# Kernel tuning notes

Hardware: AMD Instinct MI355X
Metric: run time of the kernel (lower is better)

## Reference

```python
import jax, jax.numpy as jnp
import numpy as np

N, E, ET = 50000, 400000, 50000
F, ED, H, L = 64, 32, 128, 2


def _forward(x, edge_attr, target_edge_attr, node_W, node_b, edge_W, edge_b,
             pre_W, pre_b, post_W, post_b, lin_W, lin_b, bn_g, bn_b,
             em1_W, em1_b, em2_W, em2_b, edge_index):
    n = x.shape[0]
    h = node_W.shape[1]
    src, dst = edge_index[0], edge_index[1]
    x = x @ node_W + node_b                      # [N,H]
    ea = edge_attr @ edge_W + edge_b             # [E,H]
    tea = target_edge_attr @ edge_W + edge_b     # [Et,H]

    ones = jnp.ones((src.shape[0],), jnp.float32)
    cnt = jax.ops.segment_sum(ones, dst, num_segments=n)        # in-degree per node
    avg_deg_log = jnp.mean(jnp.log(cnt + 1.0))                  # PyG avg_deg['log'] from deg histogram
    deg = jnp.clip(cnt, 1.0)[:, None]
    amp = jnp.log(deg + 1.0) / avg_deg_log                      # 'amplification' scaler
    att = avg_deg_log / jnp.log(deg + 1.0)                      # 'attenuation' scaler
    cnt_c = jnp.clip(cnt, 1.0)[:, None]
    has = (cnt > 0)[:, None]

    nlayers = pre_W.shape[0]
    for i in range(nlayers):
        # pre-MLP on message cat([x_i(dst), x_j(src), edge_attr]); split matmul avoids [E,3H] concat
        Wd, Ws, We = pre_W[i, :h], pre_W[i, h:2 * h], pre_W[i, 2 * h:]
        m = x[dst] @ Wd + x[src] @ Ws + ea @ We + pre_b[i]      # [E,H]
        s = jax.ops.segment_sum(m, dst, num_segments=n)
        mean = s / cnt_c
        mean2 = jax.ops.segment_sum(m * m, dst, num_segments=n) / cnt_c
        std = jnp.sqrt(jax.nn.relu(mean2 - mean * mean) + 1e-5)  # PyG StdAggregation
        mn = jnp.where(has, jax.ops.segment_min(m, dst, num_segments=n), 0.0)
        mx = jnp.where(has, jax.ops.segment_max(m, dst, num_segments=n), 0.0)
        agg = jnp.concatenate([mean, mn, mx, std], axis=-1)     # [N,4H] aggregator order
        scaled = jnp.concatenate([agg, agg * amp, agg * att], axis=-1)  # [N,12H] scaler order
        # post-MLP on cat([x, scaled]); split matmul
        out = x @ post_W[i, :h] + scaled @ post_W[i, h:] + post_b[i]
        out = out @ lin_W[i] + lin_b[i]
        # BatchNorm (training mode, biased var, eps=1e-5)
        mu = out.mean(axis=0)
        var = jnp.mean((out - mu) ** 2, axis=0)
        bn = bn_g[i] * (out - mu) / jnp.sqrt(var + 1e-5) + bn_b[i]
        x = (x + jax.nn.relu(bn)) / 2
        # edge update: ea + MLP(cat([x[src], x[dst], ea])) / 2
        W1s, W1d, W1e = em1_W[i, :h], em1_W[i, h:2 * h], em1_W[i, 2 * h:]
        hid = jax.nn.relu(x[src] @ W1s + x[dst] @ W1d + ea @ W1e + em1_b[i])
        ea = ea + (hid @ em2_W[i] + em2_b[i]) / 2
    return (x, ea, tea)


def setup_inputs() -> dict:
    key = jax.random.key(0)
    ks = jax.random.split(key, 24)

    def w(k, shape):
        fan_in = shape[-2]
        return (jax.random.normal(k, shape, jnp.float32) / np.sqrt(fan_in)).astype(jnp.float32)

    inp = {
        'x': jax.random.normal(ks[0], (N, F), jnp.float32),
        'edge_attr': jax.random.normal(ks[1], (E, ED), jnp.float32),
        'target_edge_attr': jax.random.normal(ks[2], (ET, ED), jnp.float32),
        'node_W': w(ks[3], (F, H)), 'node_b': jnp.zeros((H,), jnp.float32),
        'edge_W': w(ks[4], (ED, H)), 'edge_b': jnp.zeros((H,), jnp.float32),
        'pre_W': w(ks[5], (L, 3 * H, H)), 'pre_b': jnp.zeros((L, H), jnp.float32),
        'post_W': w(ks[6], (L, 13 * H, H)), 'post_b': jnp.zeros((L, H), jnp.float32),
        'lin_W': w(ks[7], (L, H, H)), 'lin_b': jnp.zeros((L, H), jnp.float32),
        'bn_g': jnp.ones((L, H), jnp.float32), 'bn_b': jnp.zeros((L, H), jnp.float32),
        'em1_W': w(ks[8], (L, 3 * H, H)), 'em1_b': jnp.zeros((L, H), jnp.float32),
        'em2_W': w(ks[9], (L, H, H)), 'em2_b': jnp.zeros((L, H), jnp.float32),
        'edge_index': jax.random.randint(ks[10], (2, E), 0, N, dtype=jnp.int32),
    }
    return inp


def reference(x, edge_attr, target_edge_attr, node_W, node_b, edge_W, edge_b,
              pre_W, pre_b, post_W, post_b, lin_W, lin_b, bn_g, bn_b,
              em1_W, em1_b, em2_W, em2_b, edge_index):
    return _forward(x, edge_attr, target_edge_attr, node_W, node_b, edge_W, edge_b,
                    pre_W, pre_b, post_W, post_b, lin_W, lin_b, bn_g, bn_b,
                    em1_W, em1_b, em2_W, em2_b, edge_index)
```

## Files before the change

### kernel.cpp

```cpp
#include <hip/hip_runtime.h>
#include <math.h>

#define NN  50000
#define NE  400000
#define NTE 50000
#define FIN 64
#define EDIM 32
#define HD  128
#define NL  2
#define SCAN_B ((NN + 255) / 256)

typedef __attribute__((ext_vector_type(8))) short bf16x8;
typedef __attribute__((ext_vector_type(4))) short bf16x4;
typedef __attribute__((ext_vector_type(4))) float f32x4;

static __device__ __forceinline__ unsigned short f2bf(float f) {
    unsigned u = __float_as_uint(f);
    unsigned r = (u + 0x7fffu + ((u >> 16) & 1u)) >> 16;
    return (unsigned short)r;
}
static __device__ __forceinline__ float bfhi2f(unsigned u) { return __uint_as_float(u & 0xffff0000u); }
static __device__ __forceinline__ float bflo2f(unsigned u) { return __uint_as_float(u << 16); }

static __device__ __forceinline__ bf16x8 load_a8(const float* p, bool ok) {
    bf16x8 a = {};
    if (ok) {
        const float4 v0 = *(const float4*)(p);
        const float4 v1 = *(const float4*)(p + 4);
        a[0] = (short)f2bf(v0.x); a[1] = (short)f2bf(v0.y);
        a[2] = (short)f2bf(v0.z); a[3] = (short)f2bf(v0.w);
        a[4] = (short)f2bf(v1.x); a[5] = (short)f2bf(v1.y);
        a[6] = (short)f2bf(v1.z); a[7] = (short)f2bf(v1.w);
    }
    return a;
}
static __device__ __forceinline__ bf16x8 pack8(float4 a, float4 b) {
    bf16x8 v;
    v[0]=(short)f2bf(a.x); v[1]=(short)f2bf(a.y); v[2]=(short)f2bf(a.z); v[3]=(short)f2bf(a.w);
    v[4]=(short)f2bf(b.x); v[5]=(short)f2bf(b.y); v[6]=(short)f2bf(b.z); v[7]=(short)f2bf(b.w);
    return v;
}
static __device__ __forceinline__ bf16x4 pack4(float4 a) {
    bf16x4 v;
    v[0]=(short)f2bf(a.x); v[1]=(short)f2bf(a.y); v[2]=(short)f2bf(a.z); v[3]=(short)f2bf(a.w);
    return v;
}

__global__ void __launch_bounds__(256) k_packW(const float* __restrict__ W,
        unsigned short* __restrict__ out, int K)
{
    const int tid = blockIdx.x * 256 + threadIdx.x;
    const int total = (K / 32) * 512;
    if (tid >= total) return;
    const int lane = tid & 63, nt = (tid >> 6) & 7, kb = tid >> 9;
    const int k0 = kb * 32 + (lane >> 4) * 8;
    const int col = nt * 16 + (lane & 15);
    bf16x8 v;
    #pragma unroll
    for (int j = 0; j < 8; ++j)
        v[j] = (short)f2bf(W[(size_t)(k0 + j) * HD + col]);
    *(bf16x8*)(out + (size_t)tid * 8) = v;
}

template<int KB>
__global__ void __launch_bounds__(256) k_gemm_mfma(const float* A,
        const unsigned short* __restrict__ Wpk, const float* __restrict__ bias,
        float* C, int M)
{
    const int t = threadIdx.x, w = t >> 6, l = t & 63;
    const int row0 = blockIdx.x * 64 + w * 16;
    const int ar = row0 + (l & 15);
    const bool aok = ar < M;
    const int kq = (l >> 4) * 8;
    const int K = KB * 32;
    f32x4 acc[8] = {};
    #pragma unroll
    for (int kb = 0; kb < KB; ++kb) {
        const bf16x8 a = load_a8(A + (size_t)ar * K + kb * 32 + kq, aok);
        #pragma unroll
        for (int nt = 0; nt < 8; ++nt) {
            const bf16x8 b = *(const bf16x8*)(Wpk + (((size_t)(kb * 8 + nt) * 64 + l) << 3));
            acc[nt] = __builtin_amdgcn_mfma_f32_16x16x32_bf16(a, b, acc[nt], 0, 0, 0);
        }
    }
    #pragma unroll
    for (int nt = 0; nt < 8; ++nt) {
        const int col = nt * 16 + (l & 15);
        const float bv = bias ? bias[col] : 0.f;
        #pragma unroll
        for (int r = 0; r < 4; ++r) {
            const int orow = row0 + (l >> 4) * 4 + r;
            if (orow < M) C[(size_t)orow * HD + col] = acc[nt][r] + bv;
        }
    }
}

template<int KB>
__global__ void __launch_bounds__(256) k_gemm2_mfma(const float* A,
        const unsigned short* __restrict__ W0, const unsigned short* __restrict__ W1,
        const float* __restrict__ b0, float* C0, float* C1, int M)
{
    const int t = threadIdx.x, w = t >> 6, l = t & 63;
    const int row0 = blockIdx.x * 64 + w * 16;
    const int ar = row0 + (l & 15);
    const bool aok = ar < M;
    const int kq = (l >> 4) * 8;
    const int K = KB * 32;
    f32x4 a0[8] = {}, a1[8] = {};
    #pragma unroll
    for (int kb = 0; kb < KB; ++kb) {
        const bf16x8 a = load_a8(A + (size_t)ar * K + kb * 32 + kq, aok);
        #pragma unroll
        for (int nt = 0; nt < 8; ++nt) {
            const bf16x8 u = *(const bf16x8*)(W0 + (((size_t)(kb * 8 + nt) * 64 + l) << 3));
            const bf16x8 v = *(const bf16x8*)(W1 + (((size_t)(kb * 8 + nt) * 64 + l) << 3));
            a0[nt] = __builtin_amdgcn_mfma_f32_16x16x32_bf16(a, u, a0[nt], 0, 0, 0);
            a1[nt] = __builtin_amdgcn_mfma_f32_16x16x32_bf16(a, v, a1[nt], 0, 0, 0);
        }
    }
    #pragma unroll
    for (int nt = 0; nt < 8; ++nt) {
        const int col = nt * 16 + (l & 15);
        const float bv = b0 ? b0[col] : 0.f;
        #pragma unroll
        for (int r = 0; r < 4; ++r) {
            const int orow = row0 + (l >> 4) * 4 + r;
            if (orow < M) {
                C0[(size_t)orow * HD + col] = a0[nt][r] + bv;
                C1[(size_t)orow * HD + col] = a1[nt][r];
            }
        }
    }
}

__global__ void __launch_bounds__(256) k_count(const int* __restrict__ d, int* __restrict__ cnt, int E)
{
    const int e = blockIdx.x * 256 + threadIdx.x;
    if (e < E) atomicAdd(&cnt[d[e]], 1);
}

__global__ void __launch_bounds__(256) k_avglog(const int* __restrict__ cnt, float* __restrict__ stats)
{
    float s = 0.f;
    for (int n = blockIdx.x * 256 + threadIdx.x; n < NN; n += gridDim.x * 256)
        s += logf((float)cnt[n] + 1.f);
    #pragma unroll
    for (int off = 32; off > 0; off >>= 1) s += __shfl_down(s, off);
    __shared__ float ls[4];
    if ((threadIdx.x & 63) == 0) ls[threadIdx.x >> 6] = s;
    __syncthreads();
    if (threadIdx.x == 0) unsafeAtomicAdd(stats, ls[0] + ls[1] + ls[2] + ls[3]);
}

__global__ void __launch_bounds__(256) k_scan_block(const int* __restrict__ cnt,
        int* __restrict__ incl, int* __restrict__ part)
{
    __shared__ int s[256];
    const int t = threadIdx.x;
    const int i = blockIdx.x * 256 + t;
    const int v = (i < NN) ? cnt[i] : 0;
    s[t] = v;
    __syncthreads();
    #pragma unroll
    for (int off = 1; off < 256; off <<= 1) {
        const int x = (t >= off) ? s[t - off] : 0;
        __syncthreads();
        s[t] += x;
        __syncthreads();
    }
    if (i < NN) incl[i] = s[t];
    if (t == 255) part[blockIdx.x] = s[255];
}

__global__ void __launch_bounds__(256) k_scan_part(const int* __restrict__ part,
        int* __restrict__ poff, int np)
{
    __shared__ int s[256];
    const int t = threadIdx.x;
    const int v = (t < np) ? part[t] : 0;
    s[t] = v;
    __syncthreads();
    #pragma unroll
    for (int off = 1; off < 256; off <<= 1) {
        const int x = (t >= off) ? s[t - off] : 0;
        __syncthreads();
        s[t] += x;
        __syncthreads();
    }
    poff[t] = s[t] - v;
}

__global__ void __launch_bounds__(256) k_scan_add(const int* __restrict__ incl,
        const int* __restrict__ cnt, const int* __restrict__ poff,
        int* __restrict__ row_start, int* __restrict__ cursor)
{
    const int i = blockIdx.x * 256 + threadIdx.x;
    if (i < NN) {
        const int excl = incl[i] - cnt[i] + poff[blockIdx.x];
        row_start[i] = excl;
        cursor[i] = excl;
    }
    if (i == 0) row_start[NN] = NE;
}

__global__ void __launch_bounds__(256) k_scatter(const int* __restrict__ dstp,
        int* cursor, int* __restrict__ sppos)
{
    const int e = blockIdx.x * 256 + threadIdx.x;
    if (e < NE) sppos[e] = atomicAdd(&cursor[dstp[e]], 1);
}

__global__ void __launch_bounds__(256) k_msg_T(const float* __restrict__ ea,
        const unsigned short* __restrict__ Wepk, const float* __restrict__ xs,
        const int* __restrict__ srcp, const int* __restrict__ sppos,
        unsigned short* __restrict__ mbuf)
{
    const int t = threadIdx.x, w = t >> 6, l = t & 63;
    const int e = blockIdx.x * 64 + w * 16 + (l & 15);
    const int q = l >> 4, kq = q * 8;
    f32x4 acc[8] = {};
    #pragma unroll
    for (int kb = 0; kb < 4; ++kb) {
        const bf16x8 bea = load_a8(ea + (size_t)e * HD + kb * 32 + kq, true);
        #pragma unroll
        for (int nt = 0; nt < 8; ++nt) {
            const bf16x8 aW = *(const bf16x8*)(Wepk + (((size_t)(kb * 8 + nt) * 64 + l) << 3));
            acc[nt] = __builtin_amdgcn_mfma_f32_16x16x32_bf16(aW, bea, acc[nt], 0, 0, 0);
        }
    }
    const int sn = srcp[e], sp = sppos[e];
    const float* ps = xs + (size_t)sn * HD + q * 4;
    unsigned short* pm = mbuf + (size_t)sp * HD + q * 4;
    #pragma unroll
    for (int nt = 0; nt < 8; ++nt) {
        const float4 sv = *(const float4*)(ps + nt * 16);
        float4 o;
        o.x = acc[nt][0] + sv.x; o.y = acc[nt][1] + sv.y;
        o.z = acc[nt][2] + sv.z; o.w = acc[nt][3] + sv.w;
        *(bf16x4*)(pm + nt * 16) = pack4(o);
    }
}

__global__ void __launch_bounds__(256) k_agg(const unsigned short* __restrict__ mbuf,
        const int* __restrict__ rs, const float* __restrict__ xd,
        unsigned short* __restrict__ aggb)
{
    const int n = blockIdx.x * 4 + (threadIdx.x >> 6);
    if (n >= NN) return;
    const int lane = threadIdx.x & 63;
    const int c = lane * 2;
    const int s = rs[n], e = rs[n + 1];
    const float2 xv = *(const float2*)(xd + (size_t)n * HD + c);
    float s0=0.f, s1=0.f, q0=0.f, q1=0.f;
    float mn0=INFINITY, mn1=INFINITY, mx0=-INFINITY, mx1=-INFINITY;
    for (int i = s; i < e; ++i) {
        const unsigned u = *(const unsigned*)(mbuf + (size_t)i * HD + c);
        const float v0 = bflo2f(u), v1 = bfhi2f(u);
        s0 += v0; s1 += v1;
        q0 += v0 * v0; q1 += v1 * v1;
        mn0 = fminf(mn0, v0); mn1 = fminf(mn1, v1);
        mx0 = fmaxf(mx0, v0); mx1 = fmaxf(mx1, v1);
    }
    const int deg = e - s;
    const float inv = 1.f / (float)(deg > 1 ? deg : 1);
    const float fd = (float)deg * inv;
    const float m0p = s0 * inv, m1p = s1 * inv;
    const float sd0 = sqrtf(fmaxf(q0 * inv - m0p * m0p, 0.f) + 1e-5f);
    const float sd1 = sqrtf(fmaxf(q1 * inv - m1p * m1p, 0.f) + 1e-5f);
    const bool has = deg > 0;
    const float mean0 = m0p + fd * xv.x, mean1 = m1p + fd * xv.y;
    const float omn0 = has ? mn0 + xv.x : 0.f, omn1 = has ? mn1 + xv.y : 0.f;
    const float omx0 = has ? mx0 + xv.x : 0.f, omx1 = has ? mx1 + xv.y : 0.f;
    unsigned* a = (unsigned*)(aggb + (size_t)n * 512 + c);
    a[0]         = (unsigned)f2bf(mean0) | ((unsigned)f2bf(mean1) << 16);
    *(a + 64)    = (unsigned)f2bf(omn0)  | ((unsigned)f2bf(omn1)  << 16);
    *(a + 128)   = (unsigned)f2bf(omx0)  | ((unsigned)f2bf(omx1)  << 16);
    *(a + 192)   = (unsigned)f2bf(sd0)   | ((unsigned)f2bf(sd1)   << 16);
}

__global__ void __launch_bounds__(256) k_post_lin(const float* __restrict__ x,
        const unsigned short* __restrict__ aggb, const int* __restrict__ cnt,
        const float* __restrict__ stats, const unsigned short* __restrict__ PWpk,
        const float* __restrict__ pb, const unsigned short* __restrict__ LNpk,
        const float* __restrict__ lb, float* __restrict__ outb, int M)
{
    __shared__ float s_amp[64], s_att[64];
    __shared__ unsigned short s_o16[64 * 128];
    const int t = threadIdx.x;
    const int row0b = blockIdx.x * 64;
    if (t < 64) {
        const int n = row0b + t;
        const float cf = (n < M) ? (float)cnt[n] : 1.f;
        const float avg = stats[0] * (1.f / (float)NN);
        const float lg = logf(fmaxf(cf, 1.f) + 1.f);
        s_amp[t] = lg / avg;
        s_att[t] = avg / lg;
    }
    __syncthreads();
    const int w = t >> 6, l = t & 63;
    const int row0 = row0b + w * 16;
    const int ar = row0 + (l & 15);
    const bool aok = ar < M;
    const int kq = (l >> 4) * 8;
    const int colb = l & 15;
    f32x4 aA[8] = {}, aB[8] = {}, aC[8] = {};

    #pragma unroll
    for (int kb = 0; kb < 4; ++kb) {
        const bf16x8 a = load_a8(x + (size_t)ar * HD + kb * 32 + kq, aok);
        #pragma unroll
        for (int nt = 0; nt < 8; ++nt) {
            const bf16x8 b = *(const bf16x8*)(PWpk + (((size_t)(kb * 8 + nt) * 64 + l) << 3));
            aA[nt] = __builtin_amdgcn_mfma_f32_16x16x32_bf16(a, b, aA[nt], 0, 0, 0);
        }
    }
    for (int jb = 0; jb < 4; ++jb) {
        #pragma unroll
        for (int k2 = 0; k2 < 4; ++k2) {
            bf16x8 a = {};
            if (aok) a = *(const bf16x8*)(aggb + (size_t)ar * 512 + jb * 128 + k2 * 32 + kq);
            const int kb1 = 4  + jb * 4 + k2;
            const int kb2 = 20 + jb * 4 + k2;
            const int kb3 = 36 + jb * 4 + k2;
            #pragma unroll
            for (int nt = 0; nt < 8; ++nt) {
                const bf16x8 b1 = *(const bf16x8*)(PWpk + (((size_t)(kb1 * 8 + nt) * 64 + l) << 3));
                const bf16x8 b2 = *(const bf16x8*)(PWpk + (((size_t)(kb2 * 8 + nt) * 64 + l) << 3));
                const bf16x8 b3 = *(const bf16x8*)(PWpk + (((size_t)(kb3 * 8 + nt) * 64 + l) << 3));
                aA[nt] = __builtin_amdgcn_mfma_f32_16x16x32_bf16(a, b1, aA[nt], 0, 0, 0);
                aB[nt] = __builtin_amdgcn_mfma_f32_16x16x32_bf16(a, b2, aB[nt], 0, 0, 0);
                aC[nt] = __builtin_amdgcn_mfma_f32_16x16x32_bf16(a, b3, aC[nt], 0, 0, 0);
            }
        }
    }
    #pragma unroll
    for (int nt = 0; nt < 8; ++nt) {
        const int col = nt * 16 + colb;
        const float bv = pb[col];
        #pragma unroll
        for (int r = 0; r < 4; ++r) {
            const int lr = w * 16 + (l >> 4) * 4 + r;
            const float o = aA[nt][r] + s_amp[lr] * aB[nt][r] + s_att[lr] * aC[nt][r] + bv;
            const int ba = lr * 256 + ((((col >> 3)) ^ (lr & 7)) << 4) + ((col & 7) << 1);
            *(unsigned short*)((char*)s_o16 + ba) = f2bf(o);
        }
    }
    __syncthreads();
    f32x4 lacc[8] = {};
    const int lrow = w * 16 + (l & 15);
    #pragma unroll
    for (int kb = 0; kb < 4; ++kb) {
        const int slot = kb * 4 + (l >> 4);
        const int ba = lrow * 256 + ((slot ^ (lrow & 7)) << 4);
        const bf16x8 a = *(const bf16x8*)((const char*)s_o16 + ba);
        #pragma unroll
        for (int nt = 0; nt < 8; ++nt) {
            const bf16x8 b = *(const bf16x8*)(LNpk + (((size_t)(kb * 8 + nt) * 64 + l) << 3));
            lacc[nt] = __builtin_amdgcn_mfma_f32_16x16x32_bf16(a, b, lacc[nt], 0, 0, 0);
        }
    }
    #pragma unroll
    for (int nt = 0; nt < 8; ++nt) {
        const int col = nt * 16 + colb;
        const float bv = lb[col];
        #pragma unroll
        for (int r = 0; r < 4; ++r) {
            const int orow = row0b + w * 16 + (l >> 4) * 4 + r;
            if (orow < M) outb[(size_t)orow * HD + col] = lacc[nt][r] + bv;
        }
    }
}

__global__ void __launch_bounds__(256) k_bnstats(const float* __restrict__ ob,
        float* __restrict__ bs, float* __restrict__ bq, int M)
{
    const int c = threadIdx.x & 127;
    const int gsub = threadIdx.x >> 7;
    float s = 0.f, qq = 0.f;
    for (int rr = blockIdx.x * 2 + gsub; rr < M; rr += gridDim.x * 2) {
        const float v = ob[(size_t)rr * HD + c];
        s += v; qq += v * v;
    }
    __shared__ float ls[2][HD], lq[2][HD];
    ls[gsub][c] = s; lq[gsub][c] = qq;
    __syncthreads();
    if (gsub == 0) {
        unsafeAtomicAdd(&bs[c], ls[0][c] + ls[1][c]);
        unsafeAtomicAdd(&bq[c], lq[0][c] + lq[1][c]);
    }
}

__global__ void __launch_bounds__(256) k_xupdate(float* x, const float* __restrict__ ob,
        const float* __restrict__ bs, const float* __restrict__ bq,
        const float* __restrict__ g, const float* __restrict__ bb)
{
    const int i = blockIdx.x * 256 + threadIdx.x;
    const int c0 = (i & 31) * 4;
    const float4 ov = ((const float4*)ob)[i];
    const float4 xv = ((const float4*)x)[i];
    const float o[4]  = {ov.x, ov.y, ov.z, ov.w};
    const float xo[4] = {xv.x, xv.y, xv.z, xv.w};
    float res[4];
    #pragma unroll
    for (int j = 0; j < 4; ++j) {
        const int c = c0 + j;
        const float mu  = bs[c] * (1.f / (float)NN);
        const float var = bq[c] * (1.f / (float)NN) - mu * mu;
        const float bn  = g[c] * (o[j] - mu) * rsqrtf(var + 1e-5f) + bb[c];
        res[j] = (xo[j] + fmaxf(bn, 0.f)) * 0.5f;
    }
    ((float4*)x)[i] = make_float4(res[0], res[1], res[2], res[3]);
}

__global__ void __launch_bounds__(256) k_edge_upd_T(float* ea,
        const unsigned short* __restrict__ W1epk, const unsigned short* __restrict__ e2pk,
        const float* __restrict__ e2b, const float* __restrict__ xs1,
        const float* __restrict__ xd1, const int* __restrict__ srcp,
        const int* __restrict__ dstp)
{
    __shared__ unsigned short s_hid[64 * 128];
    __shared__ float s_b2[128];
    const int t = threadIdx.x, w = t >> 6, l = t & 63;
    const int row0b = blockIdx.x * 64;
    if (t < 128) s_b2[t] = e2b[t];
    const int el = w * 16 + (l & 15);
    const int e = row0b + el;
    const int q = l >> 4, kq = q * 8;
    f32x4 acc1[8] = {};
    #pragma unroll
    for (int kb = 0; kb < 4; ++kb) {
        const bf16x8 bea = load_a8(ea + (size_t)e * HD + kb * 32 + kq, true);
        #pragma unroll
        for (int nt = 0; nt < 8; ++nt) {
            const bf16x8 aW = *(const bf16x8*)(W1epk + (((size_t)(kb * 8 + nt) * 64 + l) << 3));
            acc1[nt] = __builtin_amdgcn_mfma_f32_16x16x32_bf16(aW, bea, acc1[nt], 0, 0, 0);
        }
    }
    {
        const int sn = srcp[e], dn = dstp[e];
        const float* ps = xs1 + (size_t)sn * HD + q * 4;
        const float* pd = xd1 + (size_t)dn * HD + q * 4;
        #pragma unroll
        for (int nt = 0; nt < 8; ++nt) {
            const float4 sv = *(const float4*)(ps + nt * 16);
            const float4 dv = *(const float4*)(pd + nt * 16);
            float4 h;
            h.x = fmaxf(acc1[nt][0] + sv.x + dv.x, 0.f);
            h.y = fmaxf(acc1[nt][1] + sv.y + dv.y, 0.f);
            h.z = fmaxf(acc1[nt][2] + sv.z + dv.z, 0.f);
            h.w = fmaxf(acc1[nt][3] + sv.w + dv.w, 0.f);
            const int bcol = nt * 32 + q * 8;
            const int slot = bcol >> 4;
            const int ba = el * 256 + ((slot ^ (el & 7)) << 4) + (bcol & 15);
            *(bf16x4*)((char*)s_hid + ba) = pack4(h);
        }
    }
    __syncthreads();
    f32x4 acc2[8] = {};
    #pragma unroll
    for (int kb = 0; kb < 4; ++kb) {
        const int slot = kb * 4 + q;
        const int ba = el * 256 + ((slot ^ (el & 7)) << 4);
        const bf16x8 bh = *(const bf16x8*)((const char*)s_hid + ba);
        #pragma unroll
        for (int nt = 0; nt < 8; ++nt) {
            const bf16x8 aW = *(const bf16x8*)(e2pk + (((size_t)(kb * 8 + nt) * 64 + l) << 3));
            acc2[nt] = __builtin_amdgcn_mfma_f32_16x16x32_bf16(aW, bh, acc2[nt], 0, 0, 0);
        }
    }
    {
        float* pe = ea + (size_t)e * HD + q * 4;
        #pragma unroll
        for (int nt = 0; nt < 8; ++nt) {
            const float4 eo = *(const float4*)(pe + nt * 16);
            const float4 bv = *(const float4*)(&s_b2[nt * 16 + q * 4]);
            float4 o;
            o.x = eo.x + (acc2[nt][0] + bv.x) * 0.5f;
            o.y = eo.y + (acc2[nt][1] + bv.y) * 0.5f;
            o.z = eo.z + (acc2[nt][2] + bv.z) * 0.5f;
            o.w = eo.w + (acc2[nt][3] + bv.w) * 0.5f;
            *(float4*)(pe + nt * 16) = o;
        }
    }
}

extern "C" void kernel_launch(void* const* d_in, const int* in_sizes, int n_in,
                              void* d_out, int out_size, void* d_ws, size_t ws_size,
                              hipStream_t stream)
{
    const float* x0    = (const float*)d_in[0];
    const float* eatr  = (const float*)d_in[1];
    const float* teatr = (const float*)d_in[2];
    const float* nodeW = (const float*)d_in[3];
    const float* nodeb = (const float*)d_in[4];
    const float* edgeW = (const float*)d_in[5];
    const float* edgeb = (const float*)d_in[6];
    const float* preW  = (const float*)d_in[7];
    const float* preb  = (const float*)d_in[8];
    const float* postW = (const float*)d_in[9];
    const float* postb = (const float*)d_in[10];
    const float* linW  = (const float*)d_in[11];
    const float* linb  = (const float*)d_in[12];
    const float* bng   = (const float*)d_in[13];
    const float* bnb   = (const float*)d_in[14];
    const float* em1W  = (const float*)d_in[15];
    const float* em1b  = (const float*)d_in[16];
    const float* em2W  = (const float*)d_in[17];
    const float* em2b  = (const float*)d_in[18];
    const int*   eidx  = (const int*)d_in[19];
    const int* srcp = eidx;
    const int* dstp = eidx + NE;

    float* out_x  = (float*)d_out;
    float* out_ea = out_x + (size_t)NN * HD;
    float* out_te = out_ea + (size_t)NE * HD;

    const size_t NH = (size_t)NN * HD;
    const size_t EH = (size_t)NE * HD;
    float* xd   = (float*)d_ws;
    float* xs   = xd + NH;
    float* outb = xs + NH;
    float* stats = outb + NH;
    int*   cnt      = (int*)(stats + 512);
    int*   row_start = cnt + NN;
    int*   cursor   = row_start + NN + 1;
    int*   tmpincl  = cursor + NN;
    int*   part     = tmpincl + NN;
    int*   poff     = part + 256;
    int*   sppos    = poff + 256;
    unsigned short* mbuf = (unsigned short*)(((uintptr_t)(sppos + NE) + 15) & ~(uintptr_t)15);
    unsigned short* aggb = mbuf + EH;
    unsigned short* pk   = aggb + (size_t)NN * 512;
    const size_t KBSZ = 512 * 8;
    unsigned short* pkPost = pk;
    unsigned short* pkPre  = pkPost + 104 * KBSZ;
    unsigned short* pkEm1  = pkPre  + 24 * KBSZ;
    unsigned short* pkLin  = pkEm1  + 24 * KBSZ;
    unsigned short* pkEm2  = pkLin  + 8 * KBSZ;
    unsigned short* pkNode = pkEm2  + 8 * KBSZ;
    unsigned short* pkEdge = pkNode + 2 * KBSZ;

    hipMemsetAsync(cnt, 0, NN * sizeof(int), stream);
    hipMemsetAsync(stats, 0, 512 * sizeof(float), stream);

    k_packW<<<208, 256, 0, stream>>>(postW, pkPost, 3328);
    k_packW<<<48, 256, 0, stream>>>(preW,  pkPre,  768);
    k_packW<<<48, 256, 0, stream>>>(em1W,  pkEm1,  768);
    k_packW<<<16, 256, 0, stream>>>(linW,  pkLin,  256);
    k_packW<<<16, 256, 0, stream>>>(em2W,  pkEm2,  256);
    k_packW<<<4, 256, 0, stream>>>(nodeW, pkNode, 64);
    k_packW<<<2, 256, 0, stream>>>(edgeW, pkEdge, 32);

    k_gemm_mfma<1><<<(NE + 63) / 64, 256, 0, stream>>>(eatr, pkEdge, edgeb, out_ea, NE);
    k_gemm_mfma<1><<<(NTE + 63) / 64, 256, 0, stream>>>(teatr, pkEdge, edgeb, out_te, NTE);
    k_gemm_mfma<2><<<(NN + 63) / 64, 256, 0, stream>>>(x0, pkNode, nodeb, out_x, NN);

    k_count<<<(NE + 255) / 256, 256, 0, stream>>>(dstp, cnt, NE);
    k_avglog<<<256, 256, 0, stream>>>(cnt, stats);
    k_scan_block<<<SCAN_B, 256, 0, stream>>>(cnt, tmpincl, part);
    k_scan_part<<<1, 256, 0, stream>>>(part, poff, SCAN_B);
    k_scan_add<<<SCAN_B, 256, 0, stream>>>(tmpincl, cnt, poff, row_start, cursor);
    k_scatter<<<(NE + 255) / 256, 256, 0, stream>>>(dstp, cursor, sppos);

    const int gn = (NN + 63) / 64;
    const int ge = NE / 64;

    for (int l = 0; l < NL; ++l) {
        const unsigned short* Wd_pk  = pkPre + (size_t)(l * 12 + 0) * KBSZ;
        const unsigned short* Ws_pk  = pkPre + (size_t)(l * 12 + 4) * KBSZ;
        const unsigned short* We_pk  = pkPre + (size_t)(l * 12 + 8) * KBSZ;
        const unsigned short* W1s_pk = pkEm1 + (size_t)(l * 12 + 0) * KBSZ;
        const unsigned short* W1d_pk = pkEm1 + (size_t)(l * 12 + 4) * KBSZ;
        const unsigned short* W1e_pk = pkEm1 + (size_t)(l * 12 + 8) * KBSZ;
        const unsigned short* PW_pk  = pkPost + (size_t)l * 52 * KBSZ;
        const unsigned short* lin_pk = pkLin + (size_t)l * 4 * KBSZ;
        const unsigned short* em2_pk = pkEm2 + (size_t)l * 4 * KBSZ;
        const float* pbl = preb + l * HD;
        const float* pob = postb + l * HD;
        const float* lb  = linb + l * HD;
        const float* g_  = bng + l * HD;
        const float* b_  = bnb + l * HD;
        const float* e1b = em1b + l * HD;
        const float* e2b = em2b + l * HD;

        hipMemsetAsync(stats + 128, 0, 256 * sizeof(float), stream);

        k_gemm2_mfma<4><<<gn, 256, 0, stream>>>(out_x, Wd_pk, Ws_pk, pbl, xd, xs, NN);
        k_msg_T<<<ge, 256, 0, stream>>>(out_ea, We_pk, xs, srcp, sppos, mbuf);
        k_agg<<<(NN + 3) / 4, 256, 0, stream>>>(mbuf, row_start, xd, aggb);
        k_post_lin<<<gn, 256, 0, stream>>>(out_x, aggb, cnt, stats, PW_pk, pob, lin_pk, lb, outb, NN);
        k_bnstats<<<256, 256, 0, stream>>>(outb, stats + 128, stats + 256, NN);
        k_xupdate<<<NN * 32 / 256, 256, 0, stream>>>(out_x, outb, stats + 128, stats + 256, g_, b_);
        k_gemm2_mfma<4><<<gn, 256, 0, stream>>>(out_x, W1d_pk, W1s_pk, e1b, xd, xs, NN);
        k_edge_upd_T<<<ge, 256, 0, stream>>>(out_ea, W1e_pk, em2_pk, e2b, xs, xd, srcp, dstp);
    }
}
```

Before: 1.506 ms.

## Transpose MFMA operands for vectorized stores and pre-scale aggregates in agg kernel

Swaps the MFMA operand roles in the node/edge GEMMs and the post-MLP kernel so each lane holds four consecutive output columns of one row. This allows float4 stores instead of scattered scalar stores. The agg kernel now applies the amplification and attenuation scalers itself and writes a 12H-wide bf16 buffer. The post kernel therefore runs a single 52-block K loop with one accumulator set instead of three, which lowers register pressure. The cost is three times more aggregate buffer traffic per node and extra bf16 rounding of the scaled values.

New measurement: 1.454 ms. 1.04x faster.

```diff
diff --git a/kernel.cpp b/kernel.cpp
--- a/kernel.cpp
+++ b/kernel.cpp
@@ -34,12 +34,6 @@
     }
     return a;
 }
-static __device__ __forceinline__ bf16x8 pack8(float4 a, float4 b) {
-    bf16x8 v;
-    v[0]=(short)f2bf(a.x); v[1]=(short)f2bf(a.y); v[2]=(short)f2bf(a.z); v[3]=(short)f2bf(a.w);
-    v[4]=(short)f2bf(b.x); v[5]=(short)f2bf(b.y); v[6]=(short)f2bf(b.z); v[7]=(short)f2bf(b.w);
-    return v;
-}
 static __device__ __forceinline__ bf16x4 pack4(float4 a) {
     bf16x4 v;
     v[0]=(short)f2bf(a.x); v[1]=(short)f2bf(a.y); v[2]=(short)f2bf(a.z); v[3]=(short)f2bf(a.w);
@@ -63,72 +57,74 @@
 }
 
 template<int KB>
-__global__ void __launch_bounds__(256) k_gemm_mfma(const float* A,
+__global__ void __launch_bounds__(256) k_gemm_T(const float* A,
         const unsigned short* __restrict__ Wpk, const float* __restrict__ bias,
         float* C, int M)
 {
     const int t = threadIdx.x, w = t >> 6, l = t & 63;
-    const int row0 = blockIdx.x * 64 + w * 16;
-    const int ar = row0 + (l & 15);
-    const bool aok = ar < M;
-    const int kq = (l >> 4) * 8;
+    const int n = blockIdx.x * 64 + w * 16 + (l & 15);
+    const bool ok = n < M;
+    const int q = l >> 4;
     const int K = KB * 32;
     f32x4 acc[8] = {};
     #pragma unroll
     for (int kb = 0; kb < KB; ++kb) {
-        const bf16x8 a = load_a8(A + (size_t)ar * K + kb * 32 + kq, aok);
-        #pragma unroll
-        for (int nt = 0; nt < 8; ++nt) {
-            const bf16x8 b = *(const bf16x8*)(Wpk + (((size_t)(kb * 8 + nt) * 64 + l) << 3));
-            acc[nt] = __builtin_amdgcn_mfma_f32_16x16x32_bf16(a, b, acc[nt], 0, 0, 0);
-        }
-    }
-    #pragma unroll
-    for (int nt = 0; nt < 8; ++nt) {
-        const int col = nt * 16 + (l & 15);
-        const float bv = bias ? bias[col] : 0.f;
-        #pragma unroll
-        for (int r = 0; r < 4; ++r) {
-            const int orow = row0 + (l >> 4) * 4 + r;
-            if (orow < M) C[(size_t)orow * HD + col] = acc[nt][r] + bv;
+        const bf16x8 b = load_a8(A + (size_t)n * K + kb * 32 + q * 8, ok);
+        #pragma unroll
+        for (int nt = 0; nt < 8; ++nt) {
+            const bf16x8 aW = *(const bf16x8*)(Wpk + (((size_t)(kb * 8 + nt) * 64 + l) << 3));
+            acc[nt] = __builtin_amdgcn_mfma_f32_16x16x32_bf16(aW, b, acc[nt], 0, 0, 0);
+        }
+    }
+    if (ok) {
+        float* pc = C + (size_t)n * HD + q * 4;
+        #pragma unroll
+        for (int nt = 0; nt < 8; ++nt) {
+            const int col = nt * 16 + q * 4;
+            float4 bv = bias ? *(const float4*)(bias + col) : make_float4(0.f,0.f,0.f,0.f);
+            float4 o;
+            o.x = acc[nt][0] + bv.x; o.y = acc[nt][1] + bv.y;
+            o.z = acc[nt][2] + bv.z; o.w = acc[nt][3] + bv.w;
+            *(float4*)(pc + nt * 16) = o;
         }
     }
 }
 
 template<int KB>
-__global__ void __launch_bounds__(256) k_gemm2_mfma(const float* A,
+__global__ void __launch_bounds__(256) k_gemm2_T(const float* A,
         const unsigned short* __restrict__ W0, const unsigned short* __restrict__ W1,
         const float* __restrict__ b0, float* C0, float* C1, int M)
 {
     const int t = threadIdx.x, w = t >> 6, l = t & 63;
-    const int row0 = blockIdx.x * 64 + w * 16;
-    const int ar = row0 + (l & 15);
-    const bool aok = ar < M;
-    const int kq = (l >> 4) * 8;
+    const int n = blockIdx.x * 64 + w * 16 + (l & 15);
+    const bool ok = n < M;
+    const int q = l >> 4;
     const int K = KB * 32;
     f32x4 a0[8] = {}, a1[8] = {};
     #pragma unroll
     for (int kb = 0; kb < KB; ++kb) {
-        const bf16x8 a = load_a8(A + (size_t)ar * K + kb * 32 + kq, aok);
+        const bf16x8 b = load_a8(A + (size_t)n * K + kb * 32 + q * 8, ok);
         #pragma unroll
         for (int nt = 0; nt < 8; ++nt) {
             const bf16x8 u = *(const bf16x8*)(W0 + (((size_t)(kb * 8 + nt) * 64 + l) << 3));
             const bf16x8 v = *(const bf16x8*)(W1 + (((size_t)(kb * 8 + nt) * 64 + l) << 3));
-            a0[nt] = __builtin_amdgcn_mfma_f32_16x16x32_bf16(a, u, a0[nt], 0, 0, 0);
-            a1[nt] = __builtin_amdgcn_mfma_f32_16x16x32_bf16(a, v, a1[nt], 0, 0, 0);
-        }
-    }
-    #pragma unroll
-    for (int nt = 0; nt < 8; ++nt) {
-        const int col = nt * 16 + (l & 15);
-        const float bv = b0 ? b0[col] : 0.f;
-        #pragma unroll
-        for (int r = 0; r < 4; ++r) {
-            const int orow = row0 + (l >> 4) * 4 + r;
-            if (orow < M) {
-                C0[(size_t)orow * HD + col] = a0[nt][r] + bv;
-                C1[(size_t)orow * HD + col] = a1[nt][r];
-            }
+            a0[nt] = __builtin_amdgcn_mfma_f32_16x16x32_bf16(u, b, a0[nt], 0, 0, 0);
+            a1[nt] = __builtin_amdgcn_mfma_f32_16x16x32_bf16(v, b, a1[nt], 0, 0, 0);
+        }
+    }
+    if (ok) {
+        float* p0 = C0 + (size_t)n * HD + q * 4;
+        float* p1 = C1 + (size_t)n * HD + q * 4;
+        #pragma unroll
+        for (int nt = 0; nt < 8; ++nt) {
+            const int col = nt * 16 + q * 4;
+            float4 bv = b0 ? *(const float4*)(b0 + col) : make_float4(0.f,0.f,0.f,0.f);
+            float4 o0, o1;
+            o0.x = a0[nt][0] + bv.x; o0.y = a0[nt][1] + bv.y;
+            o0.z = a0[nt][2] + bv.z; o0.w = a0[nt][3] + bv.w;
+            o1.x = a1[nt][0]; o1.y = a1[nt][1]; o1.z = a1[nt][2]; o1.w = a1[nt][3];
+            *(float4*)(p0 + nt * 16) = o0;
+            *(float4*)(p1 + nt * 16) = o1;
         }
     }
 }
@@ -243,7 +239,7 @@
 
 __global__ void __launch_bounds__(256) k_agg(const unsigned short* __restrict__ mbuf,
         const int* __restrict__ rs, const float* __restrict__ xd,
-        unsigned short* __restrict__ aggb)
+        const float* __restrict__ stats, unsigned short* __restrict__ aggb)
 {
     const int n = blockIdx.x * 4 + (threadIdx.x >> 6);
     if (n >= NN) return;
@@ -268,105 +264,89 @@
     const float sd0 = sqrtf(fmaxf(q0 * inv - m0p * m0p, 0.f) + 1e-5f);
     const float sd1 = sqrtf(fmaxf(q1 * inv - m1p * m1p, 0.f) + 1e-5f);
     const bool has = deg > 0;
-    const float mean0 = m0p + fd * xv.x, mean1 = m1p + fd * xv.y;
-    const float omn0 = has ? mn0 + xv.x : 0.f, omn1 = has ? mn1 + xv.y : 0.f;
-    const float omx0 = has ? mx0 + xv.x : 0.f, omx1 = has ? mx1 + xv.y : 0.f;
-    unsigned* a = (unsigned*)(aggb + (size_t)n * 512 + c);
-    a[0]         = (unsigned)f2bf(mean0) | ((unsigned)f2bf(mean1) << 16);
-    *(a + 64)    = (unsigned)f2bf(omn0)  | ((unsigned)f2bf(omn1)  << 16);
-    *(a + 128)   = (unsigned)f2bf(omx0)  | ((unsigned)f2bf(omx1)  << 16);
-    *(a + 192)   = (unsigned)f2bf(sd0)   | ((unsigned)f2bf(sd1)   << 16);
-}
-
-__global__ void __launch_bounds__(256) k_post_lin(const float* __restrict__ x,
-        const unsigned short* __restrict__ aggb, const int* __restrict__ cnt,
-        const float* __restrict__ stats, const unsigned short* __restrict__ PWpk,
+    const float v0[4] = { m0p + fd * xv.x, has ? mn0 + xv.x : 0.f,
+                          has ? mx0 + xv.x : 0.f, sd0 };
+    const float v1[4] = { m1p + fd * xv.y, has ? mn1 + xv.y : 0.f,
+                          has ? mx1 + xv.y : 0.f, sd1 };
+    const float avg = stats[0] * (1.f / (float)NN);
+    const float lg = logf(fmaxf((float)deg, 1.f) + 1.f);
+    const float amp = lg / avg, att = avg / lg;
+    unsigned* a = (unsigned*)(aggb + (size_t)n * 1536 + c);
+    #pragma unroll
+    for (int sct = 0; sct < 4; ++sct) {
+        a[sct * 64]       = (unsigned)f2bf(v0[sct])       | ((unsigned)f2bf(v1[sct]) << 16);
+        a[256 + sct * 64] = (unsigned)f2bf(v0[sct] * amp) | ((unsigned)f2bf(v1[sct] * amp) << 16);
+        a[512 + sct * 64] = (unsigned)f2bf(v0[sct] * att) | ((unsigned)f2bf(v1[sct] * att) << 16);
+    }
+}
+
+__global__ void __launch_bounds__(256) k_post_lin_T(const float* __restrict__ x,
+        const unsigned short* __restrict__ aggb, const unsigned short* __restrict__ PWpk,
         const float* __restrict__ pb, const unsigned short* __restrict__ LNpk,
         const float* __restrict__ lb, float* __restrict__ outb, int M)
 {
-    __shared__ float s_amp[64], s_att[64];
     __shared__ unsigned short s_o16[64 * 128];
-    const int t = threadIdx.x;
-    const int row0b = blockIdx.x * 64;
-    if (t < 64) {
-        const int n = row0b + t;
-        const float cf = (n < M) ? (float)cnt[n] : 1.f;
-        const float avg = stats[0] * (1.f / (float)NN);
-        const float lg = logf(fmaxf(cf, 1.f) + 1.f);
-        s_amp[t] = lg / avg;
-        s_att[t] = avg / lg;
+    const int t = threadIdx.x, w = t >> 6, l = t & 63;
+    const int el = w * 16 + (l & 15);
+    const int n = blockIdx.x * 64 + el;
+    const bool ok = n < M;
+    const int q = l >> 4;
+    f32x4 acc[8] = {};
+    #pragma unroll
+    for (int kb = 0; kb < 4; ++kb) {
+        const bf16x8 b = load_a8(x + (size_t)n * HD + kb * 32 + q * 8, ok);
+        #pragma unroll
+        for (int nt = 0; nt < 8; ++nt) {
+            const bf16x8 aW = *(const bf16x8*)(PWpk + (((size_t)(kb * 8 + nt) * 64 + l) << 3));
+            acc[nt] = __builtin_amdgcn_mfma_f32_16x16x32_bf16(aW, b, acc[nt], 0, 0, 0);
+        }
+    }
+    const unsigned short* arow = aggb + (size_t)n * 1536 + q * 8;
+    #pragma unroll 4
+    for (int kb = 4; kb < 52; ++kb) {
+        bf16x8 b = {};
+        if (ok) b = *(const bf16x8*)(arow + (size_t)(kb - 4) * 32);
+        #pragma unroll
+        for (int nt = 0; nt < 8; ++nt) {
+            const bf16x8 aW = *(const bf16x8*)(PWpk + (((size_t)(kb * 8 + nt) * 64 + l) << 3));
+            acc[nt] = __builtin_amdgcn_mfma_f32_16x16x32_bf16(aW, b, acc[nt], 0, 0, 0);
+        }
+    }
+    #pragma unroll
+    for (int nt = 0; nt < 8; ++nt) {
+        const int col = nt * 16 + q * 4;
+        const float4 bv = *(const float4*)(pb + col);
+        float4 o;
+        o.x = acc[nt][0] + bv.x; o.y = acc[nt][1] + bv.y;
+        o.z = acc[nt][2] + bv.z; o.w = acc[nt][3] + bv.w;
+        const int bcol = nt * 32 + q * 8;
+        const int slot = bcol >> 4;
+        const int ba = el * 256 + ((slot ^ (el & 7)) << 4) + (bcol & 15);
+        *(bf16x4*)((char*)s_o16 + ba) = pack4(o);
     }
     __syncthreads();
-    const int w = t >> 6, l = t & 63;
-    const int row0 = row0b + w * 16;
-    const int ar = row0 + (l & 15);
-    const bool aok = ar < M;
-    const int kq = (l >> 4) * 8;
-    const int colb = l & 15;
-    f32x4 aA[8] = {}, aB[8] = {}, aC[8] = {};
-
+    f32x4 acc2[8] = {};
     #pragma unroll
     for (int kb = 0; kb < 4; ++kb) {
-        const bf16x8 a = load_a8(x + (size_t)ar * HD + kb * 32 + kq, aok);
-        #pragma unroll
-        for (int nt = 0; nt < 8; ++nt) {
-            const bf16x8 b = *(const bf16x8*)(PWpk + (((size_t)(kb * 8 + nt) * 64 + l) << 3));
-            aA[nt] = __builtin_amdgcn_mfma_f32_16x16x32_bf16(a, b, aA[nt], 0, 0, 0);
-        }
-    }
-    for (int jb = 0; jb < 4; ++jb) {
-        #pragma unroll
-        for (int k2 = 0; k2 < 4; ++k2) {
-            bf16x8 a = {};
-            if (aok) a = *(const bf16x8*)(aggb + (size_t)ar * 512 + jb * 128 + k2 * 32 + kq);
-            const int kb1 = 4  + jb * 4 + k2;
-            const int kb2 = 20 + jb * 4 + k2;
-            const int kb3 = 36 + jb * 4 + k2;
-            #pragma unroll
-            for (int nt = 0; nt < 8; ++nt) {
-                const bf16x8 b1 = *(const bf16x8*)(PWpk + (((size_t)(kb1 * 8 + nt) * 64 + l) << 3));
-                const bf16x8 b2 = *(const bf16x8*)(PWpk + (((size_t)(kb2 * 8 + nt) * 64 + l) << 3));
-                const bf16x8 b3 = *(const bf16x8*)(PWpk + (((size_t)(kb3 * 8 + nt) * 64 + l) << 3));
-                aA[nt] = __builtin_amdgcn_mfma_f32_16x16x32_bf16(a, b1, aA[nt], 0, 0, 0);
-                aB[nt] = __builtin_amdgcn_mfma_f32_16x16x32_bf16(a, b2, aB[nt], 0, 0, 0);
-                aC[nt] = __builtin_amdgcn_mfma_f32_16x16x32_bf16(a, b3, aC[nt], 0, 0, 0);
-            }
-        }
-    }
-    #pragma unroll
-    for (int nt = 0; nt < 8; ++nt) {
-        const int col = nt * 16 + colb;
-        const float bv = pb[col];
-        #pragma unroll
-        for (int r = 0; r < 4; ++r) {
-            const int lr = w * 16 + (l >> 4) * 4 + r;
-            const float o = aA[nt][r] + s_amp[lr] * aB[nt][r] + s_att[lr] * aC[nt][r] + bv;
-            const int ba = lr * 256 + ((((col >> 3)) ^ (lr & 7)) << 4) + ((col & 7) << 1);
-            *(unsigned short*)((char*)s_o16 + ba) = f2bf(o);
-        }
-    }
-    __syncthreads();
-    f32x4 lacc[8] = {};
-    const int lrow = w * 16 + (l & 15);
-    #pragma unroll
-    for (int kb = 0; kb < 4; ++kb) {
-        const int slot = kb * 4 + (l >> 4);
-        const int ba = lrow * 256 + ((slot ^ (lrow & 7)) << 4);
-        const bf16x8 a = *(const bf16x8*)((const char*)s_o16 + ba);
-        #pragma unroll
-        for (int nt = 0; nt < 8; ++nt) {
-            const bf16x8 b = *(const bf16x8*)(LNpk + (((size_t)(kb * 8 + nt) * 64 + l) << 3));
-            lacc[nt] = __builtin_amdgcn_mfma_f32_16x16x32_bf16(a, b, lacc[nt], 0, 0, 0);
-        }
-    }
-    #pragma unroll
-    for (int nt = 0; nt < 8; ++nt) {
-        const int col = nt * 16 + colb;
-        const float bv = lb[col];
-        #pragma unroll
-        for (int r = 0; r < 4; ++r) {
-            const int orow = row0b + w * 16 + (l >> 4) * 4 + r;
-            if (orow < M) outb[(size_t)orow * HD + col] = lacc[nt][r] + bv;
+        const int slot = kb * 4 + q;
+        const int ba = el * 256 + ((slot ^ (el & 7)) << 4);
+        const bf16x8 bh = *(const bf16x8*)((const char*)s_o16 + ba);
+        #pragma unroll
+        for (int nt = 0; nt < 8; ++nt) {
+            const bf16x8 aW = *(const bf16x8*)(LNpk + (((size_t)(kb * 8 + nt) * 64 + l) << 3));
+            acc2[nt] = __builtin_amdgcn_mfma_f32_16x16x32_bf16(aW, bh, acc2[nt], 0, 0, 0);
+        }
+    }
+    if (ok) {
+        float* pc = outb + (size_t)n * HD + q * 4;
+        #pragma unroll
+        for (int nt = 0; nt < 8; ++nt) {
+            const int col = nt * 16 + q * 4;
+            const float4 bv = *(const float4*)(lb + col);
+            float4 o;
+            o.x = acc2[nt][0] + bv.x; o.y = acc2[nt][1] + bv.y;
+            o.z = acc2[nt][2] + bv.z; o.w = acc2[nt][3] + bv.w;
+            *(float4*)(pc + nt * 16) = o;
         }
     }
 }
@@ -530,7 +510,7 @@
     int*   sppos    = poff + 256;
     unsigned short* mbuf = (unsigned short*)(((uintptr_t)(sppos + NE) + 15) & ~(uintptr_t)15);
     unsigned short* aggb = mbuf + EH;
-    unsigned short* pk   = aggb + (size_t)NN * 512;
+    unsigned short* pk   = aggb + (size_t)NN * 1536;
     const size_t KBSZ = 512 * 8;
     unsigned short* pkPost = pk;
     unsigned short* pkPre  = pkPost + 104 * KBSZ;
@@ -551,9 +531,9 @@
     k_packW<<<4, 256, 0, stream>>>(nodeW, pkNode, 64);
     k_packW<<<2, 256, 0, stream>>>(edgeW, pkEdge, 32);
 
-    k_gemm_mfma<1><<<(NE + 63) / 64, 256, 0, stream>>>(eatr, pkEdge, edgeb, out_ea, NE);
-    k_gemm_mfma<1><<<(NTE + 63) / 64, 256, 0, stream>>>(teatr, pkEdge, edgeb, out_te, NTE);
-    k_gemm_mfma<2><<<(NN + 63) / 64, 256, 0, stream>>>(x0, pkNode, nodeb, out_x, NN);
+    k_gemm_T<1><<<(NE + 63) / 64, 256, 0, stream>>>(eatr, pkEdge, edgeb, out_ea, NE);
+    k_gemm_T<1><<<(NTE + 63) / 64, 256, 0, stream>>>(teatr, pkEdge, edgeb, out_te, NTE);
+    k_gemm_T<2><<<(NN + 63) / 64, 256, 0, stream>>>(x0, pkNode, nodeb, out_x, NN);
 
     k_count<<<(NE + 255) / 256, 256, 0, stream>>>(dstp, cnt, NE);
     k_avglog<<<256, 256, 0, stream>>>(cnt, stats);
@@ -585,13 +565,13 @@
 
         hipMemsetAsync(stats + 128, 0, 256 * sizeof(float), stream);
 
-        k_gemm2_mfma<4><<<gn, 256, 0, stream>>>(out_x, Wd_pk, Ws_pk, pbl, xd, xs, NN);
+        k_gemm2_T<4><<<gn, 256, 0, stream>>>(out_x, Wd_pk, Ws_pk, pbl, xd, xs, NN);
         k_msg_T<<<ge, 256, 0, stream>>>(out_ea, We_pk, xs, srcp, sppos, mbuf);
-        k_agg<<<(NN + 3) / 4, 256, 0, stream>>>(mbuf, row_start, xd, aggb);
-        k_post_lin<<<gn, 256, 0, stream>>>(out_x, aggb, cnt, stats, PW_pk, pob, lin_pk, lb, outb, NN);
+        k_agg<<<(NN + 3) / 4, 256, 0, stream>>>(mbuf, row_start, xd, stats, aggb);
+        k_post_lin_T<<<gn, 256, 0, stream>>>(out_x, aggb, PW_pk, pob, lin_pk, lb, outb, NN);
         k_bnstats<<<256, 256, 0, stream>>>(outb, stats + 128, stats + 256, NN);
         k_xupdate<<<NN * 32 / 256, 256, 0, stream>>>(out_x, outb, stats + 128, stats + 256, g_, b_);
-        k_gemm2_mfma<4><<<gn, 256, 0, stream>>>(out_x, W1d_pk, W1s_pk, e1b, xd, xs, NN);
+        k_gemm2_T<4><<<gn, 256, 0, stream>>>(out_x, W1d_pk, W1s_pk, e1b, xd, xs, NN);
         k_edge_upd_T<<<ge, 256, 0, stream>>>(out_ea, W1e_pk, em2_pk, e2b, xs, xd, srcp, dstp);
     }
 }
```
